# Kernel tuning notes

Measured on AMD Instinct MI355X. Metric: run time of the kernel, lower is better.

The kernel has to match this reference:

```python
import jax, jax.numpy as jnp
import numpy as np

B, S, H = 2, 2048, 2048
NH, NKV, D = 16, 4, 128      # heads, kv heads, head_dim
GROUPS = NH // NKV
WIN = 1024                    # sliding window
EPS = 1e-5
THETA = 10000.0
NEG = -1e9


def _rms_norm(x, w):
    # over last dim (head_dim)
    var = jnp.mean(x * x, axis=-1, keepdims=True)
    return x * jax.lax.rsqrt(var + EPS) * w


def _rotate_half(x):
    x1, x2 = jnp.split(x, 2, axis=-1)
    return jnp.concatenate([-x2, x1], axis=-1)


def _apply_rope(q, k, cos, sin):
    # q: [B,NH,S,D], k: [B,NKV,S,D], cos/sin: [B,S,D]
    c = cos[:, None, :, :]
    s = sin[:, None, :, :]
    q = q * c + _rotate_half(q) * s
    k = k * c + _rotate_half(k) * s
    return q, k


def setup_inputs() -> dict:
    key = jax.random.key(0)
    ks = jax.random.split(key, 8)
    std = 0.02
    hidden_states = jax.random.normal(ks[0], (B, S, H), dtype=jnp.float32)
    Wq = jax.random.normal(ks[1], (NH * D, H), dtype=jnp.float32) * std
    Wk = jax.random.normal(ks[2], (NKV * D, H), dtype=jnp.float32) * std
    Wv = jax.random.normal(ks[3], (NKV * D, H), dtype=jnp.float32) * std
    Wo = jax.random.normal(ks[4], (H, NH * D), dtype=jnp.float32) * std
    Wg = jax.random.normal(ks[5], (NH * D, H), dtype=jnp.float32) * std
    q_norm_w = jnp.ones((D,), dtype=jnp.float32)
    k_norm_w = jnp.ones((D,), dtype=jnp.float32)
    # RoPE tables
    inv_freq = 1.0 / (THETA ** (jnp.arange(0, D, 2, dtype=jnp.float32) / D))
    pos = jnp.arange(S, dtype=jnp.float32)
    freqs = jnp.einsum('s,d->sd', pos, inv_freq)          # [S, D/2]
    emb = jnp.concatenate([freqs, freqs], axis=-1)        # [S, D]
    cos = jnp.broadcast_to(jnp.cos(emb)[None], (B, S, D)).astype(jnp.float32)
    sin = jnp.broadcast_to(jnp.sin(emb)[None], (B, S, D)).astype(jnp.float32)
    i = jnp.arange(S)[:, None]
    j = jnp.arange(S)[None, :]
    allowed = (j <= i) & (i - j < WIN)
    attention_mask = jnp.where(allowed, 0.0, NEG).astype(jnp.float32)[None, None]  # [1,1,S,S]
    return {
        'hidden_states': hidden_states, 'cos': cos, 'sin': sin,
        'attention_mask': attention_mask,
        'Wq': Wq, 'Wk': Wk, 'Wv': Wv, 'Wo': Wo, 'Wg': Wg,
        'q_norm_w': q_norm_w, 'k_norm_w': k_norm_w,
    }


def reference(hidden_states, cos, sin, attention_mask, Wq, Wk, Wv, Wo, Wg, q_norm_w, k_norm_w):
    x = hidden_states                                  # [B,S,H]
    q = (x @ Wq.T).reshape(B, S, NH, D)
    k = (x @ Wk.T).reshape(B, S, NKV, D)
    v = (x @ Wv.T).reshape(B, S, NKV, D)
    gate = x @ Wg.T                                    # [B,S,NH*D]
    q = _rms_norm(q, q_norm_w)
    k = _rms_norm(k, k_norm_w)
    q = q.transpose(0, 2, 1, 3)                        # [B,NH,S,D]
    k = k.transpose(0, 2, 1, 3)                        # [B,NKV,S,D]
    v = v.transpose(0, 2, 1, 3)
    # local (sliding) attention layer -> RoPE applied
    q, k = _apply_rope(q, k, cos, sin)
    # GQA: repeat kv heads
    k = jnp.repeat(k, GROUPS, axis=1)                  # [B,NH,S,D]
    v = jnp.repeat(v, GROUPS, axis=1)
    scaling = D ** -0.5
    scores = jnp.einsum('bhqd,bhkd->bhqk', q, k) * scaling
    scores = scores + attention_mask                   # broadcast [1,1,S,S]
    probs = jax.nn.softmax(scores.astype(jnp.float32), axis=-1).astype(q.dtype)
    out = jnp.einsum('bhqk,bhkd->bhqd', probs, v)      # [B,NH,S,D]
    out = out.transpose(0, 2, 1, 3).reshape(B, S, NH * D)
    out = out * jax.nn.sigmoid(gate)
    return out @ Wo.T                                  # [B,S,H]
```

## Files before the change

kernel.cpp:

```cpp
#include <hip/hip_runtime.h>
#include <hip/hip_bf16.h>

#define B_    2
#define S_    2048
#define H_    2048
#define NH_   16
#define NKV_  4
#define D_    128
#define WIN_  1024

typedef __attribute__((ext_vector_type(8))) short short8;
typedef __attribute__((ext_vector_type(4))) float f32x4;

__device__ __forceinline__ void gl2lds16(const void* g, void* l) {
  __builtin_amdgcn_global_load_lds(
      (const __attribute__((address_space(1))) void*)g,
      (__attribute__((address_space(3))) void*)l, 16, 0, 0);
}

__device__ __forceinline__ unsigned short f2bf(float x) {
  union { float f; unsigned int u; } v; v.f = x;
  unsigned int r = v.u + 0x7fffu + ((v.u >> 16) & 1u);
  return (unsigned short)(r >> 16);
}
__device__ __forceinline__ float bf2f(unsigned short u) {
  union { unsigned int i; float f; } v; v.i = ((unsigned int)u) << 16; return v.f;
}

#define CVT_TOTAL 5767168L
__global__ __launch_bounds__(256) void convert_all(
    const float* __restrict__ hs, const float* __restrict__ wq,
    const float* __restrict__ wk, const float* __restrict__ wv,
    const float* __restrict__ wg, const float* __restrict__ wo,
    unsigned short* __restrict__ xb, unsigned short* __restrict__ wall,
    unsigned short* __restrict__ wob) {
  long i = (long)blockIdx.x * 256 + threadIdx.x;
  if (i >= CVT_TOTAL) return;
  const float4* src; ushort4* dst;
  if (i < 2097152)      { src = (const float4*)hs + i;                         dst = (ushort4*)xb + i; }
  else if (i < 3145728) { long j = i - 2097152; src = (const float4*)wq + j;   dst = (ushort4*)wall + j; }
  else if (i < 3407872) { long j = i - 3145728; src = (const float4*)wk + j;   dst = (ushort4*)wall + 1048576 + j; }
  else if (i < 3670016) { long j = i - 3407872; src = (const float4*)wv + j;   dst = (ushort4*)wall + 1310720 + j; }
  else if (i < 4718592) { long j = i - 3670016; src = (const float4*)wg + j;   dst = (ushort4*)wall + 1572864 + j; }
  else                  { long j = i - 4718592; src = (const float4*)wo + j;   dst = (ushort4*)wob + j; }
  float4 v = *src;
  ushort4 o; o.x = f2bf(v.x); o.y = f2bf(v.y); o.z = f2bf(v.z); o.w = f2bf(v.w);
  *dst = o;
}

#define VMCNT0 asm volatile("s_waitcnt vmcnt(0)" ::: "memory")
#define SBAR   asm volatile("s_barrier" ::: "memory")

__global__ __launch_bounds__(512, 2) void gemm_qkvg(
    const unsigned short* __restrict__ A,
    const unsigned short* __restrict__ Bm,
    unsigned short* __restrict__ C)
{
  const int KQ = 2048, NQ = 5120;
  __shared__ unsigned short As[2][256 * 64];
  __shared__ unsigned short Bs[2][320 * 64];
  const int t = threadIdx.x;
  const int lane = t & 63;
  const int wave = t >> 6;
  const int quad = lane >> 4, rl = lane & 15;
  const int bm = blockIdx.x * 256, bn = blockIdx.y * 320;
  const int wm = (wave >> 2) * 128, wn = (wave & 3) * 80;
  const int wub = (t & ~63) * 8;

#define STAGE_A_(d, k0, rd) { int cc = (rd) * 512 + t; int row = cc >> 3;      \
    int lc = (cc & 7) ^ (row & 7);                                             \
    gl2lds16(A + (long)(bm + row) * KQ + (k0) + lc * 8,                        \
             &As[d][(rd) * 4096 + wub]); }
#define STAGE_B_(d, k0, rd) { int cc = (rd) * 512 + t; int row = cc >> 3;      \
    int lc = (cc & 7) ^ (row & 7);                                             \
    gl2lds16(Bm + (long)(bn + row) * KQ + (k0) + lc * 8,                       \
             &Bs[d][(rd) * 4096 + wub]); }
#define RD_B(dst, cb, kk) { _Pragma("unroll") for (int j = 0; j < 5; j++) {    \
    int row = wn + j * 16 + rl;                                                \
    dst[j] = *(const short8*)(&Bs[cb][row * 64 + ((((kk)*4+quad)^(row&7))*8)]); } }
#define RD_A(dst, cb, kk, f0) { _Pragma("unroll") for (int f = 0; f < 4; f++) {\
    int row = wm + ((f0) + f) * 16 + rl;                                       \
    dst[f] = *(const short8*)(&As[cb][row * 64 + ((((kk)*4+quad)^(row&7))*8)]); } }
#define MM(a_, b_, f0) { __builtin_amdgcn_s_setprio(1);                        \
    _Pragma("unroll") for (int f = 0; f < 4; f++)                              \
    _Pragma("unroll") for (int j = 0; j < 5; j++)                              \
      acc[(f0)+f][j] = __builtin_amdgcn_mfma_f32_16x16x32_bf16(                \
          a_[f], b_[j], acc[(f0)+f][j], 0, 0, 0);                              \
    __builtin_amdgcn_s_setprio(0); }

  f32x4 acc[8][5];
#pragma unroll
  for (int f = 0; f < 8; f++)
#pragma unroll
    for (int j = 0; j < 5; j++) acc[f][j] = (f32x4){0.f, 0.f, 0.f, 0.f};

  STAGE_B_(0, 0, 0); STAGE_B_(0, 0, 1); STAGE_B_(0, 0, 2);
  STAGE_B_(0, 0, 3); STAGE_B_(0, 0, 4);
  STAGE_A_(0, 0, 0); STAGE_A_(0, 0, 1);
  STAGE_A_(0, 0, 2); STAGE_A_(0, 0, 3);
  VMCNT0; SBAR;

  short8 afX[4], bfrX[5], afY[4], bfrY[5];

  for (int tk = 0; tk < 32; ++tk) {
    const int c = tk & 1, d = c ^ 1;
    const int nk0 = tk * 64 + 64;
    const bool hn = tk < 31;
    RD_B(bfrX, c, 0); RD_A(afX, c, 0, 0);
    if (hn) {
      STAGE_B_(d, nk0, 0); STAGE_B_(d, nk0, 1); STAGE_B_(d, nk0, 2);
      STAGE_B_(d, nk0, 3); STAGE_B_(d, nk0, 4);
      STAGE_A_(d, nk0, 0); STAGE_A_(d, nk0, 1);
      STAGE_A_(d, nk0, 2); STAGE_A_(d, nk0, 3);
    }
    RD_A(afY, c, 0, 4);
    MM(afX, bfrX, 0);
    RD_B(bfrY, c, 1); RD_A(afX, c, 1, 0);
    MM(afY, bfrX, 4);
    RD_A(afY, c, 1, 4);
    MM(afX, bfrY, 0);
    MM(afY, bfrY, 4);
    VMCNT0; SBAR;
  }

#pragma unroll
  for (int f = 0; f < 8; f++) {
    int row0 = bm + wm + f * 16 + quad * 4;
#pragma unroll
    for (int j = 0; j < 5; j++) {
      int col = bn + wn + j * 16 + rl;
#pragma unroll
      for (int r = 0; r < 4; r++)
        C[(long)(row0 + r) * NQ + col] = f2bf(acc[f][j][r]);
    }
  }
#undef STAGE_A_
#undef STAGE_B_
#undef RD_B
#undef RD_A
#undef MM
}

template <bool OUT_BF16>
__global__ __launch_bounds__(256) void gemm_bt(
    const unsigned short* __restrict__ A,
    const unsigned short* __restrict__ Bm,
    void* __restrict__ Cv, int M, int N, int K)
{
  __shared__ unsigned short Asl[128 * 64];
  __shared__ unsigned short Bsl[128 * 64];
  const int t = threadIdx.x;
  const int lane = t & 63, wave = t >> 6;
  const int quad = lane >> 4, rl = lane & 15;
  const int bm = blockIdx.x * 128, bn = blockIdx.y * 128;
  const int wm = (wave >> 1) * 64, wn = (wave & 1) * 64;
  const int ldsbase = (t & ~63) * 8;

  f32x4 acc[4][4];
#pragma unroll
  for (int i = 0; i < 4; i++)
#pragma unroll
    for (int j = 0; j < 4; j++) acc[i][j] = (f32x4){0.f, 0.f, 0.f, 0.f};

  for (int k0 = 0; k0 < K; k0 += 64) {
#pragma unroll
    for (int i = 0; i < 4; i++) {
      int tt = i * 256 + t;
      int row = tt >> 3;
      int lc = (tt & 7) ^ (row & 7);
      gl2lds16(A + (long)(bm + row) * K + k0 + lc * 8, Asl + i * 2048 + ldsbase);
      gl2lds16(Bm + (long)(bn + row) * K + k0 + lc * 8, Bsl + i * 2048 + ldsbase);
    }
    __syncthreads();
#pragma unroll
    for (int kk = 0; kk < 2; kk++) {
      short8 af[4], bfr[4];
#pragma unroll
      for (int i = 0; i < 4; i++) {
        int row = wm + i * 16 + rl;
        af[i] = *(const short8*)(Asl + row * 64 + (((kk * 4 + quad) ^ (row & 7)) * 8));
      }
#pragma unroll
      for (int j = 0; j < 4; j++) {
        int row = wn + j * 16 + rl;
        bfr[j] = *(const short8*)(Bsl + row * 64 + (((kk * 4 + quad) ^ (row & 7)) * 8));
      }
#pragma unroll
      for (int i = 0; i < 4; i++)
#pragma unroll
        for (int j = 0; j < 4; j++)
          acc[i][j] = __builtin_amdgcn_mfma_f32_16x16x32_bf16(af[i], bfr[j], acc[i][j], 0, 0, 0);
    }
    __syncthreads();
  }
#pragma unroll
  for (int i = 0; i < 4; i++) {
    int row0 = bm + wm + i * 16 + quad * 4;
#pragma unroll
    for (int j = 0; j < 4; j++) {
      int col = bn + wn + j * 16 + rl;
#pragma unroll
      for (int r = 0; r < 4; r++) {
        if (OUT_BF16)
          ((unsigned short*)Cv)[(long)(row0 + r) * N + col] = f2bf(acc[i][j][r]);
        else
          ((float*)Cv)[(long)(row0 + r) * N + col] = acc[i][j][r];
      }
    }
  }
}

__global__ __launch_bounds__(256) void pack_and_transpose(
    const unsigned short* __restrict__ qkvg,
    const float* __restrict__ cosb, const float* __restrict__ sinb,
    const float* __restrict__ qw, const float* __restrict__ kw,
    unsigned short* __restrict__ qb, unsigned short* __restrict__ kb,
    unsigned short* __restrict__ vt)
{
  __shared__ unsigned short tile[64][136];
  int t = threadIdx.x;
  if (blockIdx.x >= 20480) {
    int blk = blockIdx.x - 20480;
    int st = blk & 31, kv = (blk >> 5) & 3, b = blk >> 7;
    int s0 = st * 64;
#pragma unroll
    for (int i = 0; i < 4; i++) {
      int idx = i * 256 + t;
      int r = idx >> 4, c = (idx & 15) * 8;
      short8 v = *(const short8*)(qkvg + (long)(b * S_ + s0 + r) * 5120 + 2560 + kv * 128 + c);
      *(short8*)(&tile[r][c]) = v;
    }
    __syncthreads();
    long vo = (long)(b * NKV_ + kv) * 128;
#pragma unroll
    for (int i = 0; i < 8; i++) {
      int idx = i * 256 + t;
      int d = idx >> 4, sc = idx & 15;
      ushort4 o;
      o.x = tile[sc * 4 + 0][d]; o.y = tile[sc * 4 + 1][d];
      o.z = tile[sc * 4 + 2][d]; o.w = tile[sc * 4 + 3][d];
      *(ushort4*)(vt + (vo + d) * S_ + s0 + sc * 4) = o;
    }
    return;
  }
  int lane = t & 63, wave = t >> 6;
  long gw = (long)blockIdx.x * 4 + wave;
  int hu = (int)(gw % 20);
  long bs = gw / 20;
  int b = (int)(bs / S_);
  int s = (int)(bs % S_);
  const unsigned short* row = qkvg + bs * 5120;

  bool isq = hu < 16;
  const unsigned short* base = isq ? (row + hu * 128) : (row + 2048 + (hu - 16) * 128);
  float x1 = bf2f(base[lane]), x2 = bf2f(base[lane + 64]);
  float ss = x1 * x1 + x2 * x2;
#pragma unroll
  for (int m = 1; m < 64; m <<= 1) ss += __shfl_xor(ss, m, 64);
  float inv = rsqrtf(ss * (1.0f / 128.0f) + 1e-5f);
  const float* w = isq ? qw : kw;
  float n1 = x1 * inv * w[lane], n2 = x2 * inv * w[lane + 64];
  const float* cp = cosb + bs * 128;
  const float* sp = sinb + bs * 128;
  float o1 = n1 * cp[lane] - n2 * sp[lane];
  float o2 = n2 * cp[lane + 64] + n1 * sp[lane + 64];
  if (isq) {
    long o = ((long)(b * NH_ + hu) * S_ + s) * 128;
    qb[o + lane] = f2bf(o1); qb[o + lane + 64] = f2bf(o2);
  } else {
    long o = ((long)(b * NKV_ + (hu - 16)) * S_ + s) * 128;
    kb[o + lane] = f2bf(o1); kb[o + lane + 64] = f2bf(o2);
  }
}

#define KSTR 136
#define VSTR 72
#define PSTR 68
__global__ __launch_bounds__(256, 3) void attn_kernel(
    const unsigned short* __restrict__ qb,
    const unsigned short* __restrict__ kbuf,
    const unsigned short* __restrict__ vt,
    const unsigned short* __restrict__ qkvg,
    unsigned short* __restrict__ aout)
{
  __shared__ unsigned short Ks[64 * KSTR];
  __shared__ unsigned short Vs[128 * VSTR];
  __shared__ unsigned short Ps[4][16 * PSTR];
  int t = threadIdx.x, lane = t & 63, wave = t >> 6;
  int quad = lane >> 4, rl = lane & 15;
  int blk = blockIdx.x;
  int qt = 31 - (blk >> 5);
  int qu = blk & 3;
  int kv = (blk >> 2) & 3;
  int b  = (blk >> 4) & 1;
  int h = kv * 4 + wave;
  int q0 = qt * 64 + qu * 16;

  const unsigned short* qhead = qb + (((long)(b * NH_ + h)) * S_) * 128;
  short8 qf[4];
#pragma unroll
  for (int ks = 0; ks < 4; ks++)
    qf[ks] = *(const short8*)(qhead + (long)(q0 + rl) * 128 + ks * 32 + quad * 8);

  f32x4 oacc[8];
#pragma unroll
  for (int j = 0; j < 8; j++) oacc[j] = (f32x4){0.f, 0.f, 0.f, 0.f};
  float m_r[4], l_r[4];
#pragma unroll
  for (int r = 0; r < 4; r++) { m_r[r] = -1e9f; l_r[r] = 0.f; }

  const unsigned short* kbase_p = kbuf + ((long)(b * NKV_ + kv)) * S_ * 128;
  const unsigned short* vbase_p = vt + ((long)(b * NKV_ + kv)) * 128 * S_;
  int t_lo = qt - 16; if (t_lo < 0) t_lo = 0;

  int kr[4], kc[4], vr[4], vc[4];
#pragma unroll
  for (int i = 0; i < 4; i++) {
    int idx = i * 256 + t;
    kr[i] = idx >> 4; kc[i] = (idx & 15) * 8;
    vr[i] = idx >> 3; vc[i] = (idx & 7) * 8;
  }

  {
    int kb0 = t_lo * 64;
    short8 kv0[4], vv0[4];
#pragma unroll
    for (int i = 0; i < 4; i++) {
      kv0[i] = *(const short8*)(kbase_p + (long)(kb0 + kr[i]) * 128 + kc[i]);
      vv0[i] = *(const short8*)(vbase_p + (long)vr[i] * S_ + kb0 + vc[i]);
    }
#pragma unroll
    for (int i = 0; i < 4; i++) {
      *(short8*)(Ks + kr[i] * KSTR + kc[i]) = kv0[i];
      *(short8*)(Vs + vr[i] * VSTR + vc[i]) = vv0[i];
    }
  }
  __syncthreads();

  const float scale = 0.08838834764831845f;
  for (int kt = t_lo; kt <= qt; ++kt) {
    int kb0 = kt * 64;
    short8 kpre[4], vpre[4];
    if (kt < qt) {
      int nb0 = kb0 + 64;
#pragma unroll
      for (int i = 0; i < 4; i++) {
        kpre[i] = *(const short8*)(kbase_p + (long)(nb0 + kr[i]) * 128 + kc[i]);
        vpre[i] = *(const short8*)(vbase_p + (long)vr[i] * S_ + nb0 + vc[i]);
      }
    }

    f32x4 sc[4];
    __builtin_amdgcn_s_setprio(1);
#pragma unroll
    for (int nt = 0; nt < 4; nt++) {
      f32x4 c0 = (f32x4){0.f, 0.f, 0.f, 0.f};
#pragma unroll
      for (int ks = 0; ks < 4; ks++) {
        short8 bfrag = *(const short8*)(Ks + (nt * 16 + rl) * KSTR + (ks * 4 + quad) * 8);
        c0 = __builtin_amdgcn_mfma_f32_16x16x32_bf16(qf[ks], bfrag, c0, 0, 0, 0);
      }
      sc[nt] = c0;
    }
    __builtin_amdgcn_s_setprio(0);

#pragma unroll
    for (int nt = 0; nt < 4; nt++)
#pragma unroll
      for (int r = 0; r < 4; r++) {
        int i_row = q0 + quad * 4 + r;
        int j_col = kb0 + nt * 16 + rl;
        bool ok = (j_col <= i_row) && (i_row - j_col < WIN_);
        sc[nt][r] = ok ? sc[nt][r] * scale : -1e9f;
      }

    float mx[4];
#pragma unroll
    for (int r = 0; r < 4; r++) {
      float m0 = fmaxf(fmaxf(sc[0][r], sc[1][r]), fmaxf(sc[2][r], sc[3][r]));
#pragma unroll
      for (int m = 1; m < 16; m <<= 1) m0 = fmaxf(m0, __shfl_xor(m0, m, 64));
      mx[r] = m0;
    }
    bool need = (mx[0] > m_r[0]) | (mx[1] > m_r[1]) |
                (mx[2] > m_r[2]) | (mx[3] > m_r[3]);
    if (__any(need)) {
#pragma unroll
      for (int r = 0; r < 4; r++) {
        float newm = fmaxf(m_r[r], mx[r]);
        float alpha = __expf(m_r[r] - newm);
        l_r[r] *= alpha;
#pragma unroll
        for (int j = 0; j < 8; j++) oacc[j][r] *= alpha;
        m_r[r] = newm;
      }
    }
#pragma unroll
    for (int r = 0; r < 4; r++) {
      float p0 = __expf(sc[0][r] - m_r[r]), p1 = __expf(sc[1][r] - m_r[r]);
      float p2 = __expf(sc[2][r] - m_r[r]), p3 = __expf(sc[3][r] - m_r[r]);
      float rs = p0 + p1 + p2 + p3;
#pragma unroll
      for (int m = 1; m < 16; m <<= 1) rs += __shfl_xor(rs, m, 64);
      l_r[r] += rs;
      unsigned short* pw = &Ps[wave][(quad * 4 + r) * PSTR];
      pw[0 * 16 + rl] = f2bf(p0);
      pw[1 * 16 + rl] = f2bf(p1);
      pw[2 * 16 + rl] = f2bf(p2);
      pw[3 * 16 + rl] = f2bf(p3);
    }

    __builtin_amdgcn_s_setprio(1);
#pragma unroll
    for (int ks2 = 0; ks2 < 2; ks2++) {
      short8 af = *(const short8*)(&Ps[wave][rl * PSTR + (ks2 * 4 + quad) * 8]);
#pragma unroll
      for (int j = 0; j < 8; j++) {
        short8 bf2 = *(const short8*)(Vs + (j * 16 + rl) * VSTR + (ks2 * 4 + quad) * 8);
        oacc[j] = __builtin_amdgcn_mfma_f32_16x16x32_bf16(af, bf2, oacc[j], 0, 0, 0);
      }
    }
    __builtin_amdgcn_s_setprio(0);

    if (kt < qt) {
      __syncthreads();
#pragma unroll
      for (int i = 0; i < 4; i++) {
        *(short8*)(Ks + kr[i] * KSTR + kc[i]) = kpre[i];
        *(short8*)(Vs + vr[i] * VSTR + vc[i]) = vpre[i];
      }
      __syncthreads();
    }
  }

#pragma unroll
  for (int r = 0; r < 4; r++) {
    int s_idx = q0 + quad * 4 + r;
    float invl = 1.0f / l_r[r];
    long rowoff = (long)(b * S_ + s_idx);
    const unsigned short* gptr = qkvg + rowoff * 5120 + 3072 + h * 128;
    unsigned short* orow = aout + rowoff * 2048 + h * 128;
#pragma unroll
    for (int j = 0; j < 8; j++) {
      int d = j * 16 + rl;
      float o = oacc[j][r] * invl;
      float g = bf2f(gptr[d]);
      o = o / (1.0f + __expf(-g));
      orow[d] = f2bf(o);
    }
  }
}

extern "C" void kernel_launch(void* const* d_in, const int* in_sizes, int n_in,
                              void* d_out, int out_size, void* d_ws, size_t ws_size,
                              hipStream_t stream) {
  (void)in_sizes; (void)n_in; (void)out_size; (void)ws_size;
  const float* hs   = (const float*)d_in[0];
  const float* cosb = (const float*)d_in[1];
  const float* sinb = (const float*)d_in[2];
  const float* Wq = (const float*)d_in[4];
  const float* Wk = (const float*)d_in[5];
  const float* Wv = (const float*)d_in[6];
  const float* Wo = (const float*)d_in[7];
  const float* Wg = (const float*)d_in[8];
  const float* qw = (const float*)d_in[9];
  const float* kw = (const float*)d_in[10];
  float* out = (float*)d_out;

  char* ws = (char*)d_ws;
  unsigned short* Xb   = (unsigned short*)ws; ws += (size_t)4096 * 2048 * 2;
  unsigned short* Wall = (unsigned short*)ws; ws += (size_t)5120 * 2048 * 2;
  unsigned short* Wob  = (unsigned short*)ws; ws += (size_t)2048 * 2048 * 2;
  unsigned short* qkvg = (unsigned short*)ws; ws += (size_t)4096 * 5120 * 2;
  unsigned short* qb   = (unsigned short*)ws; ws += (size_t)B_ * NH_ * S_ * D_ * 2;
  unsigned short* kbuf = (unsigned short*)ws; ws += (size_t)B_ * NKV_ * S_ * D_ * 2;
  unsigned short* vtb  = (unsigned short*)ws; ws += (size_t)B_ * NKV_ * S_ * D_ * 2;
  unsigned short* aout = (unsigned short*)ws; ws += (size_t)4096 * 2048 * 2;

  convert_all<<<(int)((CVT_TOTAL + 255) / 256), 256, 0, stream>>>(
      hs, Wq, Wk, Wv, Wg, Wo, Xb, Wall, Wob);
  gemm_qkvg<<<dim3(16, 16), 512, 0, stream>>>(Xb, Wall, qkvg);
  pack_and_transpose<<<20736, 256, 0, stream>>>(qkvg, cosb, sinb, qw, kw, qb, kbuf, vtb);
  attn_kernel<<<1024, 256, 0, stream>>>(qb, kbuf, vtb, qkvg, aout);
  gemm_bt<false><<<dim3(32, 16), 256, 0, stream>>>(aout, Wob, (void*)out, 4096, 2048, 2048);
}
```

Baseline: 372.8 us.

## Remap GEMM tiles per XCD, add sched barriers, use exp2 softmax and builtin bf16 convert

The QKVG GEMM block index is remapped so blocks placed on the same XCD cover neighbouring M/N tiles, aiming for better L2 reuse. Scheduling barriers are placed between the LDS reads and the MFMA groups to pin the interleaving order. The attention softmax folds log2(e) into the scale and uses exp2f in place of __expf. The hand-written bf16 rounding is swapped for the library conversion in attention. Together these aim to cut cache misses and ALU work, at the cost of restricting the compiler's scheduling freedom.

```diff
diff --git a/kernel.cpp b/kernel.cpp
--- a/kernel.cpp
+++ b/kernel.cpp
@@ -25,6 +25,10 @@
 }
 __device__ __forceinline__ float bf2f(unsigned short u) {
   union { unsigned int i; float f; } v; v.i = ((unsigned int)u) << 16; return v.f;
+}
+__device__ __forceinline__ unsigned short f2bf_c(float x) {
+  __hip_bfloat16 h = __float2bfloat16(x);
+  union { __hip_bfloat16 h; unsigned short u; } v; v.h = h; return v.u;
 }
 
 #define CVT_TOTAL 5767168L
@@ -50,6 +54,7 @@
 
 #define VMCNT0 asm volatile("s_waitcnt vmcnt(0)" ::: "memory")
 #define SBAR   asm volatile("s_barrier" ::: "memory")
+#define SB0    __builtin_amdgcn_sched_barrier(0)
 
 __global__ __launch_bounds__(512, 2) void gemm_qkvg(
     const unsigned short* __restrict__ A,
@@ -63,7 +68,10 @@
   const int lane = t & 63;
   const int wave = t >> 6;
   const int quad = lane >> 4, rl = lane & 15;
-  const int bm = blockIdx.x * 256, bn = blockIdx.y * 320;
+  const int bid = blockIdx.y * 16 + blockIdx.x;
+  const int xcd = bid & 7, q = bid >> 3;
+  const int bm = ((xcd & 3) * 4 + (q & 3)) * 256;
+  const int bn = ((xcd >> 2) * 8 + (q >> 2)) * 320;
   const int wm = (wave >> 2) * 128, wn = (wave & 3) * 80;
   const int wub = (t & ~63) * 8;
 
@@ -114,11 +122,15 @@
       STAGE_A_(d, nk0, 2); STAGE_A_(d, nk0, 3);
     }
     RD_A(afY, c, 0, 4);
+    SB0;
     MM(afX, bfrX, 0);
     RD_B(bfrY, c, 1); RD_A(afX, c, 1, 0);
+    SB0;
     MM(afY, bfrX, 4);
     RD_A(afY, c, 1, 4);
+    SB0;
     MM(afX, bfrY, 0);
+    SB0;
     MM(afY, bfrY, 4);
     VMCNT0; SBAR;
   }
@@ -337,7 +349,7 @@
   }
   __syncthreads();
 
-  const float scale = 0.08838834764831845f;
+  const float scale = 0.08838834764831845f * 1.4426950408889634f;
   for (int kt = t_lo; kt <= qt; ++kt) {
     int kb0 = kt * 64;
     short8 kpre[4], vpre[4];
@@ -388,7 +400,7 @@
 #pragma unroll
       for (int r = 0; r < 4; r++) {
         float newm = fmaxf(m_r[r], mx[r]);
-        float alpha = __expf(m_r[r] - newm);
+        float alpha = exp2f(m_r[r] - newm);
         l_r[r] *= alpha;
 #pragma unroll
         for (int j = 0; j < 8; j++) oacc[j][r] *= alpha;
@@ -397,17 +409,17 @@
     }
 #pragma unroll
     for (int r = 0; r < 4; r++) {
-      float p0 = __expf(sc[0][r] - m_r[r]), p1 = __expf(sc[1][r] - m_r[r]);
-      float p2 = __expf(sc[2][r] - m_r[r]), p3 = __expf(sc[3][r] - m_r[r]);
+      float p0 = exp2f(sc[0][r] - m_r[r]), p1 = exp2f(sc[1][r] - m_r[r]);
+      float p2 = exp2f(sc[2][r] - m_r[r]), p3 = exp2f(sc[3][r] - m_r[r]);
       float rs = p0 + p1 + p2 + p3;
 #pragma unroll
       for (int m = 1; m < 16; m <<= 1) rs += __shfl_xor(rs, m, 64);
       l_r[r] += rs;
       unsigned short* pw = &Ps[wave][(quad * 4 + r) * PSTR];
-      pw[0 * 16 + rl] = f2bf(p0);
-      pw[1 * 16 + rl] = f2bf(p1);
-      pw[2 * 16 + rl] = f2bf(p2);
-      pw[3 * 16 + rl] = f2bf(p3);
+      pw[0 * 16 + rl] = f2bf_c(p0);
+      pw[1 * 16 + rl] = f2bf_c(p1);
+      pw[2 * 16 + rl] = f2bf_c(p2);
+      pw[3 * 16 + rl] = f2bf_c(p3);
     }
 
     __builtin_amdgcn_s_setprio(1);
@@ -446,7 +458,7 @@
       float o = oacc[j][r] * invl;
       float g = bf2f(gptr[d]);
       o = o / (1.0f + __expf(-g));
-      orow[d] = f2bf(o);
+      orow[d] = f2bf_c(o);
     }
   }
 }
```

Result: no change. 379.6 us (+1.8%).
